# Optimization experiments

Measured on AMD Instinct MI355X. Metric: run time of the kernel, lower is better.

Reference implementation:

```python
import jax, jax.numpy as jnp
import numpy as np

N = 50000        # nodes
E = 1_000_000    # edges
F_IN = 128       # input features
H1, D1 = 8, 16   # layer-1 heads / per-head dim
D2 = 2           # layer-2 out dim (heads=1, concat=False)
NEG_SLOPE = 0.2  # PyG GATConv default leaky-relu slope


def setup_inputs() -> dict:
    key = jax.random.key(0)
    ks = jax.random.split(key, 10)
    x = jax.random.normal(ks[0], (N, F_IN), dtype=jnp.float32)
    edge_index = jax.random.randint(ks[1], (2, E), 0, N, dtype=jnp.int32)
    # layer 1 params: W1 maps F_IN -> H1*D1; attention vectors per head
    W1 = jax.random.normal(ks[2], (F_IN, H1 * D1), jnp.float32) * 0.1
    a_src1 = jax.random.normal(ks[3], (H1, D1), jnp.float32) * 0.1
    a_dst1 = jax.random.normal(ks[4], (H1, D1), jnp.float32) * 0.1
    b1 = jnp.zeros((H1 * D1,), jnp.float32)
    # layer 2 params: 128 -> 2, single head
    W2 = jax.random.normal(ks[5], (H1 * D1, 1 * D2), jnp.float32) * 0.1
    a_src2 = jax.random.normal(ks[6], (1, D2), jnp.float32) * 0.1
    a_dst2 = jax.random.normal(ks[7], (1, D2), jnp.float32) * 0.1
    b2 = jnp.zeros((D2,), jnp.float32)
    return {"x": x, "edge_index": edge_index,
            "W1": W1, "a_src1": a_src1, "a_dst1": a_dst1, "b1": b1,
            "W2": W2, "a_src2": a_src2, "a_dst2": a_dst2, "b2": b2}


def gat_layer(x, src, dst, W, a_s, a_d, b, concat):
    # PyG GATConv: h = xW (per head); e_ij = leaky_relu(a_s.h_j + a_d.h_i);
    # alpha = softmax over incoming edges of node i; out_i = sum alpha_ij h_j
    n = x.shape[0]
    heads, d = a_s.shape
    h = (x @ W).reshape(n, heads, d)                      # [N,H,D]
    es = jnp.einsum('nhd,hd->nh', h, a_s)                 # [N,H]
    ed = jnp.einsum('nhd,hd->nh', h, a_d)
    e = jax.nn.leaky_relu(es[src] + ed[dst], NEG_SLOPE)   # [E,H]
    m = jax.ops.segment_max(e, dst, num_segments=n)       # stable softmax max
    m = jnp.where(jnp.isfinite(m), m, 0.0)
    w = jnp.exp(e - m[dst])
    denom = jax.ops.segment_sum(w, dst, num_segments=n)
    alpha = w / (denom[dst] + 1e-16)                      # [E,H]
    out = jax.ops.segment_sum(alpha[:, :, None] * h[src], dst, num_segments=n)
    out = out.reshape(n, heads * d) if concat else out.mean(axis=1)
    return out + b


def reference(x, edge_index, W1, a_src1, a_dst1, b1, W2, a_src2, a_dst2, b2):
    n = x.shape[0]
    loops = jnp.arange(n, dtype=edge_index.dtype)         # add_self_loops (PyG default)
    src = jnp.concatenate([edge_index[0], loops])
    dst = jnp.concatenate([edge_index[1], loops])
    x1 = jax.nn.elu(gat_layer(x, src, dst, W1, a_src1, a_dst1, b1, concat=True))
    x2 = jax.nn.elu(gat_layer(x1, src, dst, W2, a_src2, a_dst2, b2, concat=False))
    return x2.mean(axis=0)                                # [2]
```

## Files before the change

### kernel.cpp

```cpp
#include <hip/hip_runtime.h>
#include <hip/hip_fp8.h>
#include <math.h>

#define NEG_SLOPE 0.2f
#define FD 128
#define H1 8
#define BSH 7
#define BWD 128
#define CAPE 3072
#define CAPC 3200
#define SCAP 3200
#define CHK 2048
#define XPAD 136
#define CURS 16
#define LOG2E 1.44269504088896f

#if defined(__has_builtin)
#if __has_builtin(__builtin_amdgcn_cvt_pk_f32_fp8) && __has_builtin(__builtin_amdgcn_cvt_pk_fp8_f32)
#define HW_FP8 1
#endif
#if __has_builtin(__builtin_amdgcn_exp2f)
#define HW_EXP2 1
#endif
#endif

typedef float v2f __attribute__((ext_vector_type(2)));
typedef short bf16x8 __attribute__((ext_vector_type(8)));
typedef float f32x4v __attribute__((ext_vector_type(4)));

__device__ inline float fexp2(float x) {
#ifdef HW_EXP2
    return __builtin_amdgcn_exp2f(x);
#else
    return exp2f(x);
#endif
}

__device__ inline unsigned char fp8_1(float v) {
#ifdef HW_FP8
    return (unsigned char)(__builtin_amdgcn_cvt_pk_fp8_f32(v, v, 0, false) & 0xff);
#else
    __hip_fp8_e4m3 q(v); return (unsigned char)q.__x;
#endif
}

template <bool HI>
__device__ inline v2f unpack2_fp8(unsigned int pk) {
#ifdef HW_FP8
    return __builtin_amdgcn_cvt_pk_f32_fp8((int)pk, HI);
#else
    __hip_fp8_e4m3 q0, q1;
    const int sh = HI ? 16 : 0;
    q0.__x = (__hip_fp8_storage_t)((pk >> sh) & 0xff);
    q1.__x = (__hip_fp8_storage_t)((pk >> (sh + 8)) & 0xff);
    v2f r; r.x = (float)q0; r.y = (float)q1;
    return r;
#endif
}

__device__ inline unsigned int pkbf2(float a, float b) {
    union { float f; unsigned u; } ua, ub;
    ua.f = a; ub.f = b;
    unsigned ra = (ua.u + 0x7FFF + ((ua.u >> 16) & 1)) >> 16;
    unsigned rb = (ub.u + 0x7FFF + ((ub.u >> 16) & 1)) >> 16;
    return (ra & 0xFFFFu) | (rb << 16);
}

__device__ inline unsigned short bf16_1(float a) {
    union { float f; unsigned u; } ua; ua.f = a;
    return (unsigned short)((ua.u + 0x7FFF + ((ua.u >> 16) & 1)) >> 16);
}


__global__ __launch_bounds__(256) void prep_kernel(
        const float* __restrict__ W1, const float* __restrict__ a_s,
        const float* __restrict__ a_d,
        unsigned short* __restrict__ W1t, unsigned short* __restrict__ wsd,
        int* __restrict__ cur, int nbk) {
    int t = blockIdx.x * 256 + threadIdx.x;
    if (t < FD * FD) {
        int k = t >> 7, n = t & 127;
        union { float f; unsigned u; } uu;
        uu.f = W1[t];
        unsigned r = (uu.u + 0x7FFF + ((uu.u >> 16) & 1)) >> 16;
        W1t[n * FD + k] = (unsigned short)r;
    }
    if (t < 16 * FD) {
        int j = t >> 7, k = t & 127;
        int head = j & 7;
        const float* av = (j < 8) ? (a_s + head * 16) : (a_d + head * 16);
        const float* wr = W1 + k * FD + head * 16;
        float v = 0.f;
        #pragma unroll
        for (int d = 0; d < 16; d++) v += wr[d] * av[d];
        v *= LOG2E;
        unsigned short hi = bf16_1(v);
        union { float f; unsigned u; } hf; hf.u = ((unsigned)hi) << 16;
        unsigned short lo = bf16_1(v - hf.f);
        wsd[j * FD + k] = hi;
        wsd[(16 + j) * FD + k] = lo;
    }
    if (t < nbk) cur[t * CURS] = t * CAPE;
}

union FusedSmem {
    struct {
        unsigned short xs[64 * XPAD];
    } g;
    int bucket[1024];
};

__global__ __launch_bounds__(256) void fused_gemm_bucketize_kernel(
        const float* __restrict__ x, const unsigned short* __restrict__ W1t,
        const unsigned short* __restrict__ wsd,
        unsigned char* __restrict__ h1, float* __restrict__ es1, float* __restrict__ ed1,
        int N, const int* __restrict__ ei, int E, int nbk,
        int* __restrict__ bkt_cursor, int* __restrict__ bkt_edges, int nchk) {
    __shared__ FusedSmem sm;
    const int tid = threadIdx.x;

    if ((int)blockIdx.x < nchk) {
        int* lcnt = sm.bucket;
        int* lbase = sm.bucket + nbk;
        for (int i = tid; i < nbk; i += 256) lcnt[i] = 0;
        __syncthreads();
        const int base = blockIdx.x * CHK;
        const int end = min(base + CHK, E);
        int info[CHK / 256];
        #pragma unroll
        for (int t = 0; t < CHK / 256; t++) {
            int i = base + tid + t * 256;
            info[t] = -1;
            if (i < end) {
                int b = ei[E + i] >> BSH;
                int r = atomicAdd(&lcnt[b], 1);
                info[t] = (r << 9) | b;
            }
        }
        __syncthreads();
        const int rot = (int)((blockIdx.x * 53u) % (unsigned)nbk);
        for (int i = tid; i < nbk; i += 256) {
            int b = i + rot; if (b >= nbk) b -= nbk;
            int c = lcnt[b];
            lbase[b] = c ? atomicAdd(&bkt_cursor[b * CURS], c) : 0;
        }
        __syncthreads();
        #pragma unroll
        for (int t = 0; t < CHK / 256; t++) {
            int i = base + tid + t * 256;
            if (info[t] >= 0) {
                int b = info[t] & 511;
                int r = info[t] >> 9;
                int pos = lbase[b] + r;
                if (pos < (b + 1) * CAPE) {
                    unsigned int src = (unsigned int)ei[i];
                    unsigned int dl = (unsigned int)(ei[E + i] & (BWD - 1));
                    bkt_edges[pos] = (int)(src | (dl << 25));
                }
            }
        }
        return;
    }

    const int tile = blockIdx.x - nchk;
    const int row0 = tile * 64;
    unsigned short* xs = sm.g.xs;

    #pragma unroll
    for (int it = 0; it < 8; ++it) {
        int idx = it * 256 + tid;
        int r   = idx >> 5;
        int c4  = idx & 31;
        int gr  = min(row0 + r, N - 1);
        float4 v = ((const float4*)(x + (size_t)gr * FD))[c4];
        unsigned int p0 = pkbf2(v.x, v.y);
        unsigned int p1 = pkbf2(v.z, v.w);
        *(unsigned int*)(xs + r * XPAD + c4 * 4) = p0;
        *(unsigned int*)(xs + r * XPAD + c4 * 4 + 2) = p1;
    }
    __syncthreads();

    const int wave = tid >> 6, lane = tid & 63;
    const int quad = lane >> 4, l16 = lane & 15;
    const int n0w = wave * 32;

    f32x4v acc[4][2];
    f32x4v acce;
    #pragma unroll
    for (int mt = 0; mt < 4; mt++)
        #pragma unroll
        for (int nt = 0; nt < 2; nt++)
            #pragma unroll
            for (int c = 0; c < 4; c++) acc[mt][nt][c] = 0.f;
    #pragma unroll
    for (int c = 0; c < 4; c++) acce[c] = 0.f;

    #pragma unroll
    for (int kt = 0; kt < 4; kt++) {
        const int kb = kt * 32 + quad * 8;
        bf16x8 a0 = *(const bf16x8*)(xs + (0 * 16 + l16) * XPAD + kb);
        bf16x8 a1 = *(const bf16x8*)(xs + (1 * 16 + l16) * XPAD + kb);
        bf16x8 a2 = *(const bf16x8*)(xs + (2 * 16 + l16) * XPAD + kb);
        bf16x8 a3 = *(const bf16x8*)(xs + (3 * 16 + l16) * XPAD + kb);
        bf16x8 b0 = *(const bf16x8*)(W1t + (n0w + 0 * 16 + l16) * FD + kb);
        bf16x8 b1 = *(const bf16x8*)(W1t + (n0w + 1 * 16 + l16) * FD + kb);
        bf16x8 bh = *(const bf16x8*)(wsd + (0 * 16 + l16) * FD + kb);
        bf16x8 bl = *(const bf16x8*)(wsd + (1 * 16 + l16) * FD + kb);
        acc[0][0] = __builtin_amdgcn_mfma_f32_16x16x32_bf16(a0, b0, acc[0][0], 0, 0, 0);
        acc[1][0] = __builtin_amdgcn_mfma_f32_16x16x32_bf16(a1, b0, acc[1][0], 0, 0, 0);
        acc[2][0] = __builtin_amdgcn_mfma_f32_16x16x32_bf16(a2, b0, acc[2][0], 0, 0, 0);
        acc[3][0] = __builtin_amdgcn_mfma_f32_16x16x32_bf16(a3, b0, acc[3][0], 0, 0, 0);
        acc[0][1] = __builtin_amdgcn_mfma_f32_16x16x32_bf16(a0, b1, acc[0][1], 0, 0, 0);
        acc[1][1] = __builtin_amdgcn_mfma_f32_16x16x32_bf16(a1, b1, acc[1][1], 0, 0, 0);
        acc[2][1] = __builtin_amdgcn_mfma_f32_16x16x32_bf16(a2, b1, acc[2][1], 0, 0, 0);
        acc[3][1] = __builtin_amdgcn_mfma_f32_16x16x32_bf16(a3, b1, acc[3][1], 0, 0, 0);
        if (wave == 0) {
            acce = __builtin_amdgcn_mfma_f32_16x16x32_bf16(a0, bh, acce, 0, 0, 0);
            acce = __builtin_amdgcn_mfma_f32_16x16x32_bf16(a0, bl, acce, 0, 0, 0);
        } else if (wave == 1) {
            acce = __builtin_amdgcn_mfma_f32_16x16x32_bf16(a1, bh, acce, 0, 0, 0);
            acce = __builtin_amdgcn_mfma_f32_16x16x32_bf16(a1, bl, acce, 0, 0, 0);
        } else if (wave == 2) {
            acce = __builtin_amdgcn_mfma_f32_16x16x32_bf16(a2, bh, acce, 0, 0, 0);
            acce = __builtin_amdgcn_mfma_f32_16x16x32_bf16(a2, bl, acce, 0, 0, 0);
        } else {
            acce = __builtin_amdgcn_mfma_f32_16x16x32_bf16(a3, bh, acce, 0, 0, 0);
            acce = __builtin_amdgcn_mfma_f32_16x16x32_bf16(a3, bl, acce, 0, 0, 0);
        }
    }

    #pragma unroll
    for (int reg = 0; reg < 4; reg++) {
        int row = row0 + wave * 16 + quad * 4 + reg;
        if (row < N) {
            float v = acce[reg];
            if (l16 < 8) es1[row * H1 + l16] = v;
            else         ed1[row * H1 + (l16 - 8)] = v;
        }
    }

    #pragma unroll
    for (int nt = 0; nt < 2; nt++) {
        const int col = n0w + nt * 16 + l16;
        #pragma unroll
        for (int mt = 0; mt < 4; mt++) {
            #pragma unroll
            for (int reg = 0; reg < 4; reg++) {
                int row = row0 + mt * 16 + quad * 4 + reg;
                if (row < N) h1[(size_t)row * FD + col] = fp8_1(acc[mt][nt][reg]);
            }
        }
    }
}

__global__ __launch_bounds__(256) void sort2_kernel(
        const int* __restrict__ bkt_cursor, const int* __restrict__ bkt_edges,
        int* __restrict__ csr_src, int* __restrict__ rowstart,
        int* __restrict__ rowend, int N) {
    __shared__ int lcnt[BWD];
    __shared__ int lcur[BWD];
    __shared__ int stage[SCAP];
    __shared__ int sorted[SCAP];
    const int b = blockIdx.x;
    const int n0 = b << BSH;
    const int nb = min(BWD, N - n0);
    const int s = b * CAPE;
    const int cnt = min(bkt_cursor[b * CURS] - s, CAPE);
    const int region = b * CAPC;
    const int tid = threadIdx.x;

    if (tid < BWD) lcnt[tid] = (tid < nb) ? 1 : 0;
    __syncthreads();
    for (int i = tid; i < cnt; i += 256) {
        int v = bkt_edges[s + i];
        stage[i] = v;
        atomicAdd(&lcnt[((unsigned int)v) >> 25], 1);
    }
    __syncthreads();
    if (tid < 64) {
        int carry = 0;
        #pragma unroll
        for (int half = 0; half < 2; half++) {
            int i = half * 64 + tid;
            int v = lcnt[i];
            int incl = v;
            #pragma unroll
            for (int off = 1; off < 64; off <<= 1) {
                int t = __shfl_up(incl, off);
                if (tid >= off) incl += t;
            }
            lcur[i] = carry + incl - v;
            carry += __shfl(incl, 63);
        }
    }
    __syncthreads();
    if (tid < nb) {
        int p = lcur[tid];
        rowstart[n0 + tid] = region + p;
        rowend[n0 + tid] = region + p + lcnt[tid];
        sorted[p] = n0 + tid;
        lcur[tid] = p + 1;
    }
    __syncthreads();
    for (int i = tid; i < cnt; i += 256) {
        int v = stage[i];
        int dl = ((unsigned int)v) >> 25;
        int src = v & 0x1FFFFFF;
        int pos = atomicAdd(&lcur[dl], 1);
        sorted[pos] = src;
    }
    __syncthreads();
    const int total = cnt + nb;
    for (int i = total + tid; i < CAPC; i += 256) sorted[i] = 0;
    __syncthreads();
    int4* dst4 = (int4*)(csr_src + region);
    const int4* src4 = (const int4*)sorted;
    for (int i = tid; i < CAPC / 4; i += 256) dst4[i] = src4[i];
}

__global__ __launch_bounds__(256) void agg1_kernel(
        const unsigned int* __restrict__ h1, const float* __restrict__ es1,
        const float* __restrict__ ed1,
        const int* __restrict__ rowstart, const int* __restrict__ rowend,
        const int* __restrict__ csr_src,
        const float* __restrict__ b1, const float* __restrict__ W2,
        const float* __restrict__ a_s2, const float* __restrict__ a_d2,
        float4* __restrict__ nd4, float* __restrict__ ed2, int N) {
    const int j = threadIdx.x;
    const int q = j & 31;
    const int h = q >> 2;
    const int sl = q & 3;
    const int bl = q & 28;
    const int n = blockIdx.x * 8 + (j >> 5);
    const bool valid = (n < N);

    int s = 0, e = 0;
    float edh = 0.f;
    if (valid) {
        s = rowstart[n];
        e = rowend[n];
        edh = ed1[(n << 3) + h];
    }
    int nbat = (e - s + 31) >> 5;
    int nmax = max(nbat, __shfl_xor(nbat, 32));

    v2f acc01 = {0.f, 0.f}, acc23 = {0.f, 0.f};
    float wsp = 0.f;
    for (int k = 0; k < nmax; ++k) {
        int base = s + (k << 5);
        int cm = min(e - base, 32);
        int myidx = csr_src[base + q];
        myidx = min(max(myidx, 0), N - 1);
        int cl = max(cm - 1, 0);
        int cmax = max(cm, __shfl_xor(cm, 32));
        for (int t = 0; t < cmax; t += 8) {
            int eA = t + sl, eB = eA + 4;
            int sA = __shfl(myidx, min(eA, cl), 32);
            int sB = __shfl(myidx, min(eB, cl), 32);
            float gA = es1[(sA << 3) + h];
            float gB = es1[(sB << 3) + h];
            int i0 = min(t, cl),     i1 = min(t + 1, cl);
            int i2 = min(t + 2, cl), i3 = min(t + 3, cl);
            int i4 = min(t + 4, cl), i5 = min(t + 5, cl);
            int i6 = min(t + 6, cl), i7 = min(t + 7, cl);
            int s0 = __shfl(myidx, i0, 32);
            int s1 = __shfl(myidx, i1, 32);
            int s2 = __shfl(myidx, i2, 32);
            int s3 = __shfl(myidx, i3, 32);
            int s4 = __shfl(myidx, i4, 32);
            int s5 = __shfl(myidx, i5, 32);
            int s6 = __shfl(myidx, i6, 32);
            int s7 = __shfl(myidx, i7, 32);
            unsigned int p0 = h1[(s0 << 5) + q];
            unsigned int p1 = h1[(s1 << 5) + q];
            unsigned int p2 = h1[(s2 << 5) + q];
            unsigned int p3 = h1[(s3 << 5) + q];
            unsigned int p4 = h1[(s4 << 5) + q];
            unsigned int p5 = h1[(s5 << 5) + q];
            unsigned int p6 = h1[(s6 << 5) + q];
            unsigned int p7 = h1[(s7 << 5) + q];
            gA += edh; gB += edh;
            gA = fmaxf(gA, gA * NEG_SLOPE);
            gB = fmaxf(gB, gB * NEG_SLOPE);
            float wA = (eA < cm) ? fexp2(gA) : 0.f;
            float wB = (eB < cm) ? fexp2(gB) : 0.f;
            wsp += wA + wB;
            float w0 = __shfl(wA, bl + 0, 32);
            float w1 = __shfl(wA, bl + 1, 32);
            float w2 = __shfl(wA, bl + 2, 32);
            float w3 = __shfl(wA, bl + 3, 32);
            float w4 = __shfl(wB, bl + 0, 32);
            float w5 = __shfl(wB, bl + 1, 32);
            float w6 = __shfl(wB, bl + 2, 32);
            float w7 = __shfl(wB, bl + 3, 32);
            v2f a01 = unpack2_fp8<false>(p0), a23 = unpack2_fp8<true>(p0);
            v2f b01 = unpack2_fp8<false>(p1), b23 = unpack2_fp8<true>(p1);
            v2f c01 = unpack2_fp8<false>(p2), c23 = unpack2_fp8<true>(p2);
            v2f d01 = unpack2_fp8<false>(p3), d23 = unpack2_fp8<true>(p3);
            v2f e01 = unpack2_fp8<false>(p4), e23 = unpack2_fp8<true>(p4);
            v2f f01 = unpack2_fp8<false>(p5), f23 = unpack2_fp8<true>(p5);
            v2f g01 = unpack2_fp8<false>(p6), g23 = unpack2_fp8<true>(p6);
            v2f h01 = unpack2_fp8<false>(p7), h23 = unpack2_fp8<true>(p7);
            acc01 += a01 * w0; acc23 += a23 * w0;
            acc01 += b01 * w1; acc23 += b23 * w1;
            acc01 += c01 * w2; acc23 += c23 * w2;
            acc01 += d01 * w3; acc23 += d23 * w3;
            acc01 += e01 * w4; acc23 += e23 * w4;
            acc01 += f01 * w5; acc23 += f23 * w5;
            acc01 += g01 * w6; acc23 += g23 * w6;
            acc01 += h01 * w7; acc23 += h23 * w7;
        }
    }

    float wsum = wsp;
    wsum += __shfl_xor(wsum, 1);
    wsum += __shfl_xor(wsum, 2);

    float inv = 1.f / wsum;
    float4 bv = *(const float4*)&b1[4 * q];
    float x0 = acc01.x * inv + bv.x;
    float x1 = acc01.y * inv + bv.y;
    float x2 = acc23.x * inv + bv.z;
    float x3 = acc23.y * inv + bv.w;
    x0 = (x0 > 0.f) ? x0 : expm1f(x0);
    x1 = (x1 > 0.f) ? x1 : expm1f(x1);
    x2 = (x2 > 0.f) ? x2 : expm1f(x2);
    x3 = (x3 > 0.f) ? x3 : expm1f(x3);

    float4 w2a = *(const float4*)&W2[8 * q];
    float4 w2b = *(const float4*)&W2[8 * q + 4];
    float c0 = x0 * w2a.x + x1 * w2a.z + x2 * w2b.x + x3 * w2b.z;
    float c1 = x0 * w2a.y + x1 * w2a.w + x2 * w2b.y + x3 * w2b.w;
    #pragma unroll
    for (int m = 1; m < 32; m <<= 1) {
        c0 += __shfl_xor(c0, m);
        c1 += __shfl_xor(c1, m);
    }
    if (q == 0 && valid) {
        float4 nv;
        nv.x = c0;
        nv.y = c1;
        nv.z = LOG2E * (c0 * a_s2[0] + c1 * a_s2[1]);
        nv.w = 0.f;
        nd4[n] = nv;
        ed2[n] = LOG2E * (c0 * a_d2[0] + c1 * a_d2[1]);
    }
}

__global__ __launch_bounds__(256) void agg2_kernel(
        const float4* __restrict__ nd4, const float* __restrict__ ed2,
        const int* __restrict__ rowstart, const int* __restrict__ rowend,
        const int* __restrict__ csr_src,
        const float* __restrict__ b2, float* __restrict__ partial, int N) {
    const int g = threadIdx.x >> 5, lane = threadIdx.x & 31;
    const int n = blockIdx.x * 8 + g;
    float v0 = 0.f, v1 = 0.f;
    if (n < N) {
        const float ed = ed2[n];
        const int s = rowstart[n], e = rowend[n];
        float a0 = 0.f, a1 = 0.f, ws = 0.f;
        for (int i = s + lane; i < e; i += 32) {
            int src = csr_src[i];
            float4 nv = nd4[src];
            float t = nv.z + ed;
            float w = fexp2(fmaxf(t, t * NEG_SLOPE));
            a0 += w * nv.x;
            a1 += w * nv.y;
            ws += w;
        }
        #pragma unroll
        for (int m = 1; m < 32; m <<= 1) {
            a0 += __shfl_xor(a0, m, 32);
            a1 += __shfl_xor(a1, m, 32);
            ws += __shfl_xor(ws, m, 32);
        }
        if (lane == 0) {
            v0 = a0 / ws + b2[0]; v0 = (v0 > 0.f) ? v0 : expm1f(v0);
            v1 = a1 / ws + b2[1]; v1 = (v1 > 0.f) ? v1 : expm1f(v1);
        }
    }
    __shared__ float buf[16];
    if (lane == 0) { buf[g * 2] = v0; buf[g * 2 + 1] = v1; }
    __syncthreads();
    if (threadIdx.x == 0) {
        float s0 = 0.f, s1 = 0.f;
        #pragma unroll
        for (int i = 0; i < 8; i++) { s0 += buf[2 * i]; s1 += buf[2 * i + 1]; }
        partial[(size_t)blockIdx.x * 2 + 0] = s0;
        partial[(size_t)blockIdx.x * 2 + 1] = s1;
    }
}

__global__ __launch_bounds__(256) void final_reduce_kernel(
        const float* __restrict__ partial, int nb, float invN, float* __restrict__ out) {
    const int tid = threadIdx.x, lane = tid & 63, wv = tid >> 6;
    float s0 = 0.f, s1 = 0.f;
    for (int i = tid; i < nb; i += 256) { s0 += partial[2 * i]; s1 += partial[2 * i + 1]; }
    #pragma unroll
    for (int m = 1; m < 64; m <<= 1) { s0 += __shfl_xor(s0, m); s1 += __shfl_xor(s1, m); }
    __shared__ float buf[8];
    if (lane == 0) { buf[wv * 2] = s0; buf[wv * 2 + 1] = s1; }
    __syncthreads();
    if (tid == 0) {
        out[0] = (buf[0] + buf[2] + buf[4] + buf[6]) * invN;
        out[1] = (buf[1] + buf[3] + buf[5] + buf[7]) * invN;
    }
}

extern "C" void kernel_launch(void* const* d_in, const int* in_sizes, int n_in,
                              void* d_out, int out_size, void* d_ws, size_t ws_size,
                              hipStream_t stream) {
    const float* x    = (const float*)d_in[0];
    const int*   ei   = (const int*)  d_in[1];
    const float* W1   = (const float*)d_in[2];
    const float* a_s1 = (const float*)d_in[3];
    const float* a_d1 = (const float*)d_in[4];
    const float* b1   = (const float*)d_in[5];
    const float* W2   = (const float*)d_in[6];
    const float* a_s2 = (const float*)d_in[7];
    const float* a_d2 = (const float*)d_in[8];
    const float* b2   = (const float*)d_in[9];
    float* out = (float*)d_out;

    const int N = in_sizes[0] / FD;
    const int E = in_sizes[1] / 2;
    const int nbk  = (N + BWD - 1) >> BSH;
    const int nchk = (E + CHK - 1) / CHK;
    const int ngemm = (N + 63) / 64;

    char* wp = (char*)d_ws;
    auto carve = [&](size_t bytes) {
        char* p = wp;
        wp += (bytes + 255) & ~(size_t)255;
        return p;
    };
    unsigned char* h1 = (unsigned char*)carve((size_t)N * FD);
    float* es1      = (float*)carve((size_t)N * H1 * 4);
    float* ed1      = (float*)carve((size_t)N * H1 * 4);
    int*   rowstart = (int*)  carve((size_t)N * 4);
    int*   rowend   = (int*)  carve((size_t)N * 4);
    int*   csr_src  = (int*)  carve(((size_t)nbk * CAPC + CAPC) * 4);
    int*   bkt_cursor = (int*)carve((size_t)nbk * CURS * 4);
    int*   bkt_edges  = (int*)carve((size_t)nbk * CAPE * 4);
    unsigned short* W1t = (unsigned short*)carve((size_t)FD * FD * 2);
    unsigned short* wsd = (unsigned short*)carve((size_t)32 * FD * 2);
    float4* nd4     = (float4*)carve((size_t)N * 16);
    float* ed2      = (float*)carve((size_t)N * 4);
    const int nb2   = (N + 7) / 8;
    float* partial  = (float*)carve((size_t)nb2 * 2 * 4);

    prep_kernel<<<(FD * FD + 255) / 256, 256, 0, stream>>>(W1, a_s1, a_d1, W1t, wsd,
                                                           bkt_cursor, nbk);

    fused_gemm_bucketize_kernel<<<nchk + ngemm, 256, 0, stream>>>(
        x, W1t, wsd, h1, es1, ed1, N, ei, E, nbk, bkt_cursor, bkt_edges, nchk);

    sort2_kernel<<<nbk, 256, 0, stream>>>(bkt_cursor, bkt_edges, csr_src, rowstart, rowend, N);

    agg1_kernel<<<(N + 7) / 8, 256, 0, stream>>>((const unsigned int*)h1, es1, ed1,
                                                 rowstart, rowend, csr_src,
                                                 b1, W2, a_s2, a_d2, nd4, ed2, N);

    agg2_kernel<<<(N + 7) / 8, 256, 0, stream>>>(nd4, ed2, rowstart, rowend, csr_src,
                                                 b2, partial, N);
    final_reduce_kernel<<<1, 256, 0, stream>>>(partial, nb2, 1.0f / (float)N, out);
}
```

Baseline: 173.6 us.

## Assign one full wavefront per node in agg1 with half-wave edge split

The layer-1 aggregation now maps one node to a 64-lane wavefront instead of a 32-lane half-wave. Each half processes alternate groups of 8 edges and the partial accumulators and weight sums are combined with a cross-half shuffle at the end. This removes the divergence between two unrelated nodes sharing a wave and adds a fast path that skips clamping and masking for full 16-edge groups. The cost is half as many nodes per block, extra reduction shuffles, and idle lanes on nodes with few edges, since average degree is about 21.

```diff
diff --git a/kernel.cpp b/kernel.cpp
--- a/kernel.cpp
+++ b/kernel.cpp
@@ -327,11 +327,13 @@
         const float* __restrict__ a_s2, const float* __restrict__ a_d2,
         float4* __restrict__ nd4, float* __restrict__ ed2, int N) {
     const int j = threadIdx.x;
-    const int q = j & 31;
+    const int lane = j & 63;
+    const int q = lane & 31;
     const int h = q >> 2;
     const int sl = q & 3;
-    const int bl = q & 28;
-    const int n = blockIdx.x * 8 + (j >> 5);
+    const int bl = (lane & 28) | (lane & 32);
+    const int half = lane >> 5;
+    const int n = blockIdx.x * 4 + (j >> 6);
     const bool valid = (n < N);
 
     int s = 0, e = 0;
@@ -341,36 +343,58 @@
         e = rowend[n];
         edh = ed1[(n << 3) + h];
     }
-    int nbat = (e - s + 31) >> 5;
-    int nmax = max(nbat, __shfl_xor(nbat, 32));
+    const int nbat = (e - s + 63) >> 6;
 
     v2f acc01 = {0.f, 0.f}, acc23 = {0.f, 0.f};
     float wsp = 0.f;
-    for (int k = 0; k < nmax; ++k) {
-        int base = s + (k << 5);
-        int cm = min(e - base, 32);
-        int myidx = csr_src[base + q];
+    for (int k = 0; k < nbat; ++k) {
+        int base = s + (k << 6);
+        int cm = min(e - base, 64);
+        int myidx = csr_src[base + lane];
         myidx = min(max(myidx, 0), N - 1);
         int cl = max(cm - 1, 0);
-        int cmax = max(cm, __shfl_xor(cm, 32));
-        for (int t = 0; t < cmax; t += 8) {
-            int eA = t + sl, eB = eA + 4;
-            int sA = __shfl(myidx, min(eA, cl), 32);
-            int sB = __shfl(myidx, min(eB, cl), 32);
-            float gA = es1[(sA << 3) + h];
-            float gB = es1[(sB << 3) + h];
-            int i0 = min(t, cl),     i1 = min(t + 1, cl);
-            int i2 = min(t + 2, cl), i3 = min(t + 3, cl);
-            int i4 = min(t + 4, cl), i5 = min(t + 5, cl);
-            int i6 = min(t + 6, cl), i7 = min(t + 7, cl);
-            int s0 = __shfl(myidx, i0, 32);
-            int s1 = __shfl(myidx, i1, 32);
-            int s2 = __shfl(myidx, i2, 32);
-            int s3 = __shfl(myidx, i3, 32);
-            int s4 = __shfl(myidx, i4, 32);
-            int s5 = __shfl(myidx, i5, 32);
-            int s6 = __shfl(myidx, i6, 32);
-            int s7 = __shfl(myidx, i7, 32);
+        for (int t = 0; t < cm; t += 16) {
+            const int te = t + half * 8;
+            int s0, s1, s2, s3, s4, s5, s6, s7, sA, sB;
+            float wA, wB;
+            if (t + 16 <= cm) {
+                sA = __shfl(myidx, te + sl);
+                sB = __shfl(myidx, te + 4 + sl);
+                s0 = __shfl(myidx, te + 0);
+                s1 = __shfl(myidx, te + 1);
+                s2 = __shfl(myidx, te + 2);
+                s3 = __shfl(myidx, te + 3);
+                s4 = __shfl(myidx, te + 4);
+                s5 = __shfl(myidx, te + 5);
+                s6 = __shfl(myidx, te + 6);
+                s7 = __shfl(myidx, te + 7);
+                float gA = es1[(sA << 3) + h];
+                float gB = es1[(sB << 3) + h];
+                gA += edh; gB += edh;
+                gA = fmaxf(gA, gA * NEG_SLOPE);
+                gB = fmaxf(gB, gB * NEG_SLOPE);
+                wA = fexp2(gA);
+                wB = fexp2(gB);
+            } else {
+                int eA = te + sl, eB = eA + 4;
+                sA = __shfl(myidx, min(eA, cl));
+                sB = __shfl(myidx, min(eB, cl));
+                s0 = __shfl(myidx, min(te + 0, cl));
+                s1 = __shfl(myidx, min(te + 1, cl));
+                s2 = __shfl(myidx, min(te + 2, cl));
+                s3 = __shfl(myidx, min(te + 3, cl));
+                s4 = __shfl(myidx, min(te + 4, cl));
+                s5 = __shfl(myidx, min(te + 5, cl));
+                s6 = __shfl(myidx, min(te + 6, cl));
+                s7 = __shfl(myidx, min(te + 7, cl));
+                float gA = es1[(sA << 3) + h];
+                float gB = es1[(sB << 3) + h];
+                gA += edh; gB += edh;
+                gA = fmaxf(gA, gA * NEG_SLOPE);
+                gB = fmaxf(gB, gB * NEG_SLOPE);
+                wA = (eA < cm) ? fexp2(gA) : 0.f;
+                wB = (eB < cm) ? fexp2(gB) : 0.f;
+            }
             unsigned int p0 = h1[(s0 << 5) + q];
             unsigned int p1 = h1[(s1 << 5) + q];
             unsigned int p2 = h1[(s2 << 5) + q];
@@ -379,20 +403,15 @@
             unsigned int p5 = h1[(s5 << 5) + q];
             unsigned int p6 = h1[(s6 << 5) + q];
             unsigned int p7 = h1[(s7 << 5) + q];
-            gA += edh; gB += edh;
-            gA = fmaxf(gA, gA * NEG_SLOPE);
-            gB = fmaxf(gB, gB * NEG_SLOPE);
-            float wA = (eA < cm) ? fexp2(gA) : 0.f;
-            float wB = (eB < cm) ? fexp2(gB) : 0.f;
             wsp += wA + wB;
-            float w0 = __shfl(wA, bl + 0, 32);
-            float w1 = __shfl(wA, bl + 1, 32);
-            float w2 = __shfl(wA, bl + 2, 32);
-            float w3 = __shfl(wA, bl + 3, 32);
-            float w4 = __shfl(wB, bl + 0, 32);
-            float w5 = __shfl(wB, bl + 1, 32);
-            float w6 = __shfl(wB, bl + 2, 32);
-            float w7 = __shfl(wB, bl + 3, 32);
+            float w0 = __shfl(wA, bl + 0);
+            float w1 = __shfl(wA, bl + 1);
+            float w2 = __shfl(wA, bl + 2);
+            float w3 = __shfl(wA, bl + 3);
+            float w4 = __shfl(wB, bl + 0);
+            float w5 = __shfl(wB, bl + 1);
+            float w6 = __shfl(wB, bl + 2);
+            float w7 = __shfl(wB, bl + 3);
             v2f a01 = unpack2_fp8<false>(p0), a23 = unpack2_fp8<true>(p0);
             v2f b01 = unpack2_fp8<false>(p1), b23 = unpack2_fp8<true>(p1);
             v2f c01 = unpack2_fp8<false>(p2), c23 = unpack2_fp8<true>(p2);
@@ -412,9 +431,14 @@
         }
     }
 
+    acc01.x += __shfl_xor(acc01.x, 32);
+    acc01.y += __shfl_xor(acc01.y, 32);
+    acc23.x += __shfl_xor(acc23.x, 32);
+    acc23.y += __shfl_xor(acc23.y, 32);
     float wsum = wsp;
     wsum += __shfl_xor(wsum, 1);
     wsum += __shfl_xor(wsum, 2);
+    wsum += __shfl_xor(wsum, 32);
 
     float inv = 1.f / wsum;
     float4 bv = *(const float4*)&b1[4 * q];
@@ -433,10 +457,10 @@
     float c1 = x0 * w2a.y + x1 * w2a.w + x2 * w2b.y + x3 * w2b.w;
     #pragma unroll
     for (int m = 1; m < 32; m <<= 1) {
-        c0 += __shfl_xor(c0, m);
-        c1 += __shfl_xor(c1, m);
-    }
-    if (q == 0 && valid) {
+        c0 += __shfl_xor(c0, m, 32);
+        c1 += __shfl_xor(c1, m, 32);
+    }
+    if (q == 0 && half == 0 && valid) {
         float4 nv;
         nv.x = c0;
         nv.y = c1;
@@ -557,7 +581,7 @@
 
     sort2_kernel<<<nbk, 256, 0, stream>>>(bkt_cursor, bkt_edges, csr_src, rowstart, rowend, N);
 
-    agg1_kernel<<<(N + 7) / 8, 256, 0, stream>>>((const unsigned int*)h1, es1, ed1,
+    agg1_kernel<<<(N + 3) / 4, 256, 0, stream>>>((const unsigned int*)h1, es1, ed1,
                                                  rowstart, rowend, csr_src,
                                                  b1, W2, a_s2, a_d2, nd4, ed2, N);
 
```

After: 182.8 us. 1.05x slower.
